# Kernel tuning notes

Measured on AMD Instinct MI355X. Metric: run time of the kernel, lower is better.

The kernel has to match this reference:

```python
import jax, jax.numpy as jnp
import numpy as np

HIDDEN = 2048
HEADS = 16
HEAD_DIM = HIDDEN // HEADS
LATENT = 512
B, T = 2, 2048


def setup_inputs() -> dict:
    key = jax.random.key(0)
    ks = jax.random.split(key, 12)
    s = lambda fan_in: 1.0 / np.sqrt(fan_in)
    x = jax.random.normal(ks[0], (B, T, HIDDEN), dtype=jnp.float32)
    Wq = jax.random.uniform(ks[1], (HIDDEN, HIDDEN), jnp.float32, -s(HIDDEN), s(HIDDEN))
    bq = jax.random.uniform(ks[2], (HIDDEN,), jnp.float32, -s(HIDDEN), s(HIDDEN))
    Wl = jax.random.uniform(ks[3], (HIDDEN, LATENT), jnp.float32, -s(HIDDEN), s(HIDDEN))
    bl = jax.random.uniform(ks[4], (LATENT,), jnp.float32, -s(HIDDEN), s(HIDDEN))
    # per-head back-projections stacked along head axis: [H, latent, head_dim]
    Wk = jax.random.uniform(ks[5], (HEADS, LATENT, HEAD_DIM), jnp.float32, -s(LATENT), s(LATENT))
    bk = jax.random.uniform(ks[6], (HEADS, HEAD_DIM), jnp.float32, -s(LATENT), s(LATENT))
    Wv = jax.random.uniform(ks[7], (HEADS, LATENT, HEAD_DIM), jnp.float32, -s(LATENT), s(LATENT))
    bv = jax.random.uniform(ks[8], (HEADS, HEAD_DIM), jnp.float32, -s(LATENT), s(LATENT))
    Wo = jax.random.uniform(ks[9], (HIDDEN, HIDDEN), jnp.float32, -s(HIDDEN), s(HIDDEN))
    bo = jax.random.uniform(ks[10], (HIDDEN,), jnp.float32, -s(HIDDEN), s(HIDDEN))
    return {"x": x, "Wq": Wq, "bq": bq, "Wl": Wl, "bl": bl,
            "Wk": Wk, "bk": bk, "Wv": Wv, "bv": bv, "Wo": Wo, "bo": bo}


def reference(x, Wq, bq, Wl, bl, Wk, bk, Wv, bv, Wo, bo):
    Bc, Tc, _ = x.shape
    # Q projection, split into heads: [B, H, T, Dh]
    q = (x @ Wq + bq).reshape(Bc, Tc, HEADS, HEAD_DIM).transpose(0, 2, 1, 3)
    # shared low-rank latent KV (cache=None -> just new tokens): [B, T, L]
    latent = x @ Wl + bl
    # per-head back-projections fused as one grouped matmul: [B, H, T, Dh]
    k = jnp.einsum('btl,hld->bhtd', latent, Wk) + bk[None, :, None, :]
    v = jnp.einsum('btl,hld->bhtd', latent, Wv) + bv[None, :, None, :]
    # full (non-causal) attention, matching the original module
    scores = jnp.einsum('bhqd,bhkd->bhqk', q, k) / np.sqrt(HEAD_DIM).astype(jnp.float32)
    probs = jax.nn.softmax(scores, axis=-1)
    attn = jnp.einsum('bhqk,bhkd->bhqd', probs, v)
    attn = attn.transpose(0, 2, 1, 3).reshape(Bc, Tc, HIDDEN)
    return attn @ Wo + bo
```

## Files before the change

### kernel.cpp

```cpp
#include <hip/hip_runtime.h>
#include <hip/hip_bf16.h>
#include <cstdint>

#define SEQ     2048
#define NHID    2048
#define NLAT    512
#define NHEAD   16
#define DHEAD   128
#define NBATCH  2
#define NROWS   (NBATCH*SEQ)

typedef unsigned short u16;
typedef __attribute__((ext_vector_type(8))) short short8;
typedef __attribute__((ext_vector_type(4))) float f32x4;

#define MFMA16 __builtin_amdgcn_mfma_f32_16x16x32_bf16

#define QSCALE 0.12751743f

#if __has_builtin(__builtin_amdgcn_exp2f)
#define EXP2(x) __builtin_amdgcn_exp2f(x)
#else
#define EXP2(x) __expf((x) * 0.6931471805599453f)
#endif

__device__ __forceinline__ u16 f2b(float f) {
    uint32_t u = __float_as_uint(f);
    uint32_t r = (u + 0x7fffu + ((u >> 16) & 1u)) >> 16;
    return (u16)r;
}

__device__ __forceinline__ uint32_t cvt_pk_bf16(float a, float b) {
    uint32_t r;
    asm("v_cvt_pk_bf16_f32 %0, %1, %2" : "=v"(r) : "v"(a), "v"(b));
    return r;
}

__device__ __forceinline__ void async16(const u16* g, u16* l) {
    __builtin_amdgcn_global_load_lds(
        (const __attribute__((address_space(1))) unsigned int*)g,
        (__attribute__((address_space(3))) unsigned int*)l, 16, 0, 0);
}

__device__ __forceinline__ void stage_lds(const u16* __restrict__ src, size_t strideE,
                                          u16* lds, int wave, int lane,
                                          int log2cpr, int xmask, int xshift,
                                          int reps, int nlanes) {
    const int cmask = (1 << log2cpr) - 1;
    for (int rep = 0; rep < reps; ++rep) {
        int cbase = rep * nlanes + wave * 64;
        int ci = cbase + lane;
        int row = ci >> log2cpr;
        int sc = ci & cmask;
        int dchunk = sc ^ ((row >> xshift) & xmask);
        const u16* g = src + (size_t)row * strideE + dchunk * 8;
        async16(g, lds + (size_t)cbase * 8);
    }
}

__global__ __launch_bounds__(256) void prep(const float* __restrict__ x,
                                            const float* __restrict__ Wq,
                                            const float* __restrict__ Wl,
                                            const float* __restrict__ Wk,
                                            const float* __restrict__ Wv,
                                            const float* __restrict__ Wo,
                                            u16* __restrict__ xb,
                                            u16* __restrict__ WqlT,
                                            u16* __restrict__ WkvT,
                                            u16* __restrict__ WoT) {
    const int t = blockIdx.x, tid = threadIdx.x;
    if (t < 8192) {
        int i = t * 256 + tid;
        float4 v = ((const float4*)x)[i];
        unsigned int lo = (unsigned int)f2b(v.x) | ((unsigned int)f2b(v.y) << 16);
        unsigned int hi = (unsigned int)f2b(v.z) | ((unsigned int)f2b(v.w) << 16);
        ((uint2*)xb)[i] = make_uint2(lo, hi);
        return;
    }
    __shared__ float tile[32][33];
    const float* src; u16* dst; int R, C, tY, tX;
    if (t < 12288)      { int tt = t - 8192;  src = Wq; dst = WqlT;           R = 2048; C = 2048; tY = tt >> 6; tX = tt & 63; }
    else if (t < 13312) { int tt = t - 12288; src = Wl; dst = WqlT + 4194304; R = 2048; C = 512;  tY = tt >> 4; tX = tt & 15; }
    else if (t < 14336) { int tt = t - 13312; int hh = tt >> 6; tt &= 63;
                          src = Wk + hh * 65536; dst = WkvT + hh * 65536;     R = 512;  C = 128;  tY = tt >> 2; tX = tt & 3; }
    else if (t < 15360) { int tt = t - 14336; int hh = tt >> 6; tt &= 63;
                          src = Wv + hh * 65536; dst = WkvT + 1048576 + hh * 65536;
                                                                              R = 512;  C = 128;  tY = tt >> 2; tX = tt & 3; }
    else                { int tt = t - 15360; src = Wo; dst = WoT;            R = 2048; C = 2048; tY = tt >> 6; tX = tt & 63; }
    const int r0 = tY * 32, c0 = tX * 32;
    {
        const int rr = tid >> 3, c4 = tid & 7;
        float4 v4 = *(const float4*)&src[(size_t)(r0 + rr) * C + c0 + c4 * 4];
        tile[rr][c4 * 4 + 0] = v4.x;
        tile[rr][c4 * 4 + 1] = v4.y;
        tile[rr][c4 * 4 + 2] = v4.z;
        tile[rr][c4 * 4 + 3] = v4.w;
    }
    __syncthreads();
    {
        const int rg = tid & 7, cc = tid >> 3;
        ushort4 o4;
        o4.x = f2b(tile[rg * 4 + 0][cc]);
        o4.y = f2b(tile[rg * 4 + 1][cc]);
        o4.z = f2b(tile[rg * 4 + 2][cc]);
        o4.w = f2b(tile[rg * 4 + 3][cc]);
        *(ushort4*)&dst[(size_t)(c0 + cc) * R + r0 + rg * 4] = o4;
    }
}

template<int STORE, int BK>
__global__ __launch_bounds__(256) void gemm_bt(const u16* __restrict__ A,
                                               const u16* __restrict__ Bt,
                                               const float* __restrict__ bias1,
                                               const float* __restrict__ bias2,
                                               void* __restrict__ C1,
                                               void* __restrict__ C2,
                                               int M, int N, int K) {
    __shared__ __align__(16) u16 As[2][128 * BK];
    __shared__ __align__(16) u16 Bs[2][128 * BK];
    const int tid = threadIdx.x, wave = tid >> 6, lane = tid & 63;
    const int quad = lane >> 4, m16 = lane & 15;
    const int gx = gridDim.x;
    const int nwg = gx * gridDim.y;
    int lin = blockIdx.x + gx * blockIdx.y;
    int xcd = lin & 7, pos = lin >> 3;
    int qq = nwg >> 3, rr2 = nwg & 7;
    int wg = (xcd < rr2) ? xcd * (qq + 1) + pos
                         : rr2 * (qq + 1) + (xcd - rr2) * qq + pos;
    const int m0 = (wg / gx) * 128, n0 = (wg % gx) * 128;
    const int wr = wave >> 1, wc = wave & 1;
    const u16* Ab = A + (size_t)m0 * K;
    const u16* Bb = Bt + (size_t)n0 * K;
    const int KI = K / BK;

    auto stage = [&](const u16* src, u16* buf) {
        if constexpr (BK == 32) stage_lds(src, K, buf, wave, lane, 2, 3, 1, 2, 256);
        else                    stage_lds(src, K, buf, wave, lane, 3, 7, 0, 4, 256);
    };

    stage(Ab, As[0]);
    stage(Bb, Bs[0]);

    f32x4 acc[4][4] = {};
    for (int it = 0; it < KI; ++it) {
        const int cur = it & 1;
        __syncthreads();
        if (it + 1 < KI) {
            stage(Ab + (it + 1) * BK, As[cur ^ 1]);
            stage(Bb + (it + 1) * BK, Bs[cur ^ 1]);
        }
        if constexpr (BK == 32) {
            const int swz = (quad ^ ((m16 >> 1) & 3)) * 8;
            short8 af[4], bfr[4];
            #pragma unroll
            for (int i = 0; i < 4; i++)
                af[i] = *(const short8*)&As[cur][(wr * 64 + i * 16 + m16) * 32 + swz];
            #pragma unroll
            for (int j = 0; j < 4; j++)
                bfr[j] = *(const short8*)&Bs[cur][(wc * 64 + j * 16 + m16) * 32 + swz];
            #pragma unroll
            for (int i = 0; i < 4; i++)
                #pragma unroll
                for (int j = 0; j < 4; j++)
                    acc[i][j] = MFMA16(af[i], bfr[j], acc[i][j], 0, 0, 0);
        } else {
            #pragma unroll
            for (int kk = 0; kk < 2; kk++) {
                const int swz = ((kk * 4 + quad) ^ (m16 & 7)) * 8;
                short8 af[4], bfr[4];
                #pragma unroll
                for (int i = 0; i < 4; i++)
                    af[i] = *(const short8*)&As[cur][(wr * 64 + i * 16 + m16) * 64 + swz];
                #pragma unroll
                for (int j = 0; j < 4; j++)
                    bfr[j] = *(const short8*)&Bs[cur][(wc * 64 + j * 16 + m16) * 64 + swz];
                #pragma unroll
                for (int i = 0; i < 4; i++)
                    #pragma unroll
                    for (int j = 0; j < 4; j++)
                        acc[i][j] = MFMA16(af[i], bfr[j], acc[i][j], 0, 0, 0);
            }
        }
    }
    const bool second = (n0 >= 2048);
    #pragma unroll
    for (int j = 0; j < 4; j++) {
        int n = n0 + wc * 64 + j * 16 + m16;
        float bv;
        if constexpr (STORE == 2) bv = bias1[n];
        else bv = second ? bias2[n - 2048] : bias1[n];
        #pragma unroll
        for (int i = 0; i < 4; i++) {
            int mrow = m0 + wr * 64 + i * 16 + quad * 4;
            if constexpr (STORE == 4) {
                if (second) {
                    int n2 = n - 2048;
                    ushort4 pkv;
                    pkv.x = f2b(acc[i][j][0] + bv);
                    pkv.y = f2b(acc[i][j][1] + bv);
                    pkv.z = f2b(acc[i][j][2] + bv);
                    pkv.w = f2b(acc[i][j][3] + bv);
                    int c = mrow & 2047;
                    c = (c & ~12) | ((c & 4) << 1) | ((c & 8) >> 1);
                    *(ushort4*)&((u16*)C2)[((size_t)((m0 >> 11) * 2048 + n2)) * 2048 + c] = pkv;
                    continue;
                }
            }
            #pragma unroll
            for (int r = 0; r < 4; r++) {
                float v = acc[i][j][r] + bv;
                int m = mrow + r;
                if constexpr (STORE == 2)
                    ((float*)C1)[(size_t)m * N + n] = v;
                else if constexpr (STORE == 3) {
                    if (!second) ((u16*)C1)[(size_t)m * 2048 + n] = f2b(v * QSCALE);
                    else         ((u16*)C2)[(size_t)m * 512 + (n - 2048)] = f2b(v);
                } else {
                    ((u16*)C1)[(size_t)m * 2048 + n] = f2b(v);
                }
            }
        }
    }
}

__global__ __launch_bounds__(256, 2) void attn_fused(const u16* __restrict__ Q,
                                                     const u16* __restrict__ Kf,
                                                     const u16* __restrict__ Vt,
                                                     u16* __restrict__ Ob) {
    __shared__ __align__(16) u16 Kt[2][64 * 128];
    __shared__ __align__(16) u16 Vtile[2][128 * 64];
    const int tid = threadIdx.x, wave = tid >> 6, lane = tid & 63;
    const int quad = lane >> 4, m16 = lane & 15;
    const int bh = blockIdx.x, b = bh >> 4, h = bh & 15;
    const int q0 = blockIdx.y * 128;
    const size_t grow = (size_t)b * SEQ;
    const u16* Kbase = Kf + grow * NHID + h * DHEAD;
    const u16* Vbase = Vt + (grow + h * DHEAD) * SEQ;

    const u16* qsrc = Q + (grow + q0) * NHID + h * DHEAD;
    stage_lds(qsrc, NHID, Kt[0], wave, lane, 4, 15, 0, 4, 256);
    stage_lds(qsrc + (size_t)64 * NHID, NHID, Kt[1], wave, lane, 4, 15, 0, 4, 256);
    __syncthreads();
    short8 qf[2][4];
    {
        const u16* qbuf = Kt[wave >> 1];
        int rbase = (wave & 1) * 32;
        #pragma unroll
        for (int i = 0; i < 2; i++)
            #pragma unroll
            for (int c = 0; c < 4; c++)
                qf[i][c] = *(const short8*)&qbuf[(rbase + i * 16 + m16) * 128 +
                                                (((c * 4 + quad) ^ m16)) * 8];
    }
    __syncthreads();

    stage_lds(Kbase, NHID, Kt[0], wave, lane, 4, 15, 0, 4, 256);
    stage_lds(Vbase, SEQ, Vtile[0], wave, lane, 3, 7, 0, 4, 256);

    f32x4 o[2][8] = {};
    float lsum[2] = {};

    for (int it = 0; it < SEQ / 64; ++it) {
        const int cur = it & 1;
        __syncthreads();
        if (it + 1 < SEQ / 64) {
            stage_lds(Kbase + (size_t)(it + 1) * 64 * NHID, NHID, Kt[cur ^ 1],
                      wave, lane, 4, 15, 0, 4, 256);
            stage_lds(Vbase + (it + 1) * 64, SEQ, Vtile[cur ^ 1],
                      wave, lane, 3, 7, 0, 4, 256);
        }
        const u16* kt = Kt[cur];
        const u16* vt = Vtile[cur];

        f32x4 s[2][4] = {};
        __builtin_amdgcn_s_setprio(1);
        #pragma unroll
        for (int c = 0; c < 4; c++)
            #pragma unroll
            for (int j = 0; j < 4; j++) {
                short8 kb = *(const short8*)&kt[(j * 16 + m16) * 128 +
                                               (((c * 4 + quad) ^ m16)) * 8];
                s[0][j] = MFMA16(kb, qf[0][c], s[0][j], 0, 0, 0);
                s[1][j] = MFMA16(kb, qf[1][c], s[1][j], 0, 0, 0);
            }
        __builtin_amdgcn_s_setprio(0);

        uint32_t pk[2][4][2];
        #pragma unroll
        for (int i = 0; i < 2; i++) {
            float rs = 0.f;
            #pragma unroll
            for (int j = 0; j < 4; j++) {
                float p0 = EXP2(s[i][j][0]);
                float p1 = EXP2(s[i][j][1]);
                float p2 = EXP2(s[i][j][2]);
                float p3 = EXP2(s[i][j][3]);
                rs += (p0 + p1) + (p2 + p3);
                pk[i][j][0] = cvt_pk_bf16(p0, p1);
                pk[i][j][1] = cvt_pk_bf16(p2, p3);
            }
            lsum[i] += rs;
        }

        __builtin_amdgcn_s_setprio(1);
        #pragma unroll
        for (int c2 = 0; c2 < 2; c2++) {
            short8 pa[2];
            #pragma unroll
            for (int i = 0; i < 2; i++) {
                union { uint32_t u[4]; short8 s8; } pu;
#if __has_builtin(__builtin_amdgcn_permlane32_swap)
                auto r0 = __builtin_amdgcn_permlane32_swap(pk[i][2 * c2][0],
                                                           pk[i][2 * c2 + 1][0],
                                                           false, false);
                auto r1 = __builtin_amdgcn_permlane32_swap(pk[i][2 * c2][1],
                                                           pk[i][2 * c2 + 1][1],
                                                           false, false);
                pu.u[0] = r0[0]; pu.u[1] = r1[0]; pu.u[2] = r0[1]; pu.u[3] = r1[1];
#else
                uint32_t jl0 = pk[i][2 * c2][0],     jl1 = pk[i][2 * c2][1];
                uint32_t jh0 = pk[i][2 * c2 + 1][0], jh1 = pk[i][2 * c2 + 1][1];
                uint32_t sl0 = __shfl_xor(jl0, 32), sl1 = __shfl_xor(jl1, 32);
                uint32_t sh0 = __shfl_xor(jh0, 32), sh1 = __shfl_xor(jh1, 32);
                const bool low = lane < 32;
                pu.u[0] = low ? jl0 : sh0;
                pu.u[1] = low ? jl1 : sh1;
                pu.u[2] = low ? sl0 : jh0;
                pu.u[3] = low ? sl1 : jh1;
#endif
                pa[i] = pu.s8;
            }
            #pragma unroll
            for (int jd = 0; jd < 8; jd++) {
                short8 vb = *(const short8*)&vt[(jd * 16 + m16) * 64 +
                                               (((c2 * 4 + quad) ^ (m16 & 7))) * 8];
                o[0][jd] = MFMA16(pa[0], vb, o[0][jd], 0, 0, 0);
                o[1][jd] = MFMA16(pa[1], vb, o[1][jd], 0, 0, 0);
            }
        }
        __builtin_amdgcn_s_setprio(0);
    }

    #pragma unroll
    for (int i = 0; i < 2; i++) {
        float v = lsum[i];
        v += __shfl_xor(v, 16);
        v += __shfl_xor(v, 32);
        lsum[i] = v;
    }
    #pragma unroll
    for (int i = 0; i < 2; i++) {
        float inv[4];
        #pragma unroll
        for (int r = 0; r < 4; r++)
            inv[r] = 1.f / __shfl(lsum[i], quad * 4 + r);
        #pragma unroll
        for (int jd = 0; jd < 8; jd++)
            #pragma unroll
            for (int r = 0; r < 4; r++) {
                int t = q0 + wave * 32 + i * 16 + quad * 4 + r;
                int d = jd * 16 + m16;
                Ob[(grow + t) * NHID + h * DHEAD + d] = f2b(o[i][jd][r] * inv[r]);
            }
    }
}

extern "C" void kernel_launch(void* const* d_in, const int* in_sizes, int n_in,
                              void* d_out, int out_size, void* d_ws, size_t ws_size,
                              hipStream_t stream) {
    const float* x  = (const float*)d_in[0];
    const float* Wq = (const float*)d_in[1];
    const float* bq = (const float*)d_in[2];
    const float* Wl = (const float*)d_in[3];
    const float* bl = (const float*)d_in[4];
    const float* Wk = (const float*)d_in[5];
    const float* bk = (const float*)d_in[6];
    const float* Wv = (const float*)d_in[7];
    const float* bv = (const float*)d_in[8];
    const float* Wo = (const float*)d_in[9];
    const float* bo = (const float*)d_in[10];
    float* out = (float*)d_out;

    u16* w = (u16*)d_ws;
    u16* xb    = w;
    u16* WqlT  = xb    + 8388608;
    u16* WkvT  = WqlT  + 5242880;
    u16* WoT   = WkvT  + 2097152;
    u16* qb    = WoT   + 4194304;
    u16* kb    = qb    + 8388608;
    u16* vt    = kb    + 8388608;
    u16* lat   = vt    + 8388608;
    u16* attnb = xb;

    prep<<<19456, 256, 0, stream>>>(x, Wq, Wl, Wk, Wv, Wo, xb, WqlT, WkvT, WoT);

    gemm_bt<3, 64><<<dim3(20, 32), 256, 0, stream>>>(xb, WqlT, bq, bl, qb, lat,
                                                     NROWS, 2560, 2048);
    gemm_bt<4, 32><<<dim3(32, 32), 256, 0, stream>>>(lat, WkvT, bk, bv, kb, vt,
                                                     NROWS, 4096, 512);

    attn_fused<<<dim3(32, 16), 256, 0, stream>>>(qb, kb, vt, attnb);

    gemm_bt<2, 64><<<dim3(16, 32), 256, 0, stream>>>(attnb, WoT, bo, nullptr, out, nullptr,
                                                     NROWS, 2048, 2048);
}
```

Before: 335.4 us.

## Halve attention tiles to 64 queries and 32 keys for higher occupancy

The attention kernel now gives each wave 16 query rows instead of 32 and streams 32-key tiles instead of 64. This halves register and LDS use, raises launch bounds to 4 blocks per CU and doubles the grid, with the V-tile swizzle adjusted to the new 32-wide layout. The cost is half the MFMA work per K/V tile load, so K/V traffic per query doubles and the kernel does twice as many barriers. Separately, the QKV GEMM's second template parameter changes from 64 to 32.

```diff
diff --git a/kernel.cpp b/kernel.cpp
--- a/kernel.cpp
+++ b/kernel.cpp
@@ -223,146 +223,128 @@
     }
 }
 
-__global__ __launch_bounds__(256, 2) void attn_fused(const u16* __restrict__ Q,
+__global__ __launch_bounds__(256, 4) void attn_fused(const u16* __restrict__ Q,
                                                      const u16* __restrict__ Kf,
                                                      const u16* __restrict__ Vt,
                                                      u16* __restrict__ Ob) {
-    __shared__ __align__(16) u16 Kt[2][64 * 128];
-    __shared__ __align__(16) u16 Vtile[2][128 * 64];
+    __shared__ __align__(16) u16 Kt[2][32 * 128];
+    __shared__ __align__(16) u16 Vtile[2][128 * 32];
     const int tid = threadIdx.x, wave = tid >> 6, lane = tid & 63;
     const int quad = lane >> 4, m16 = lane & 15;
     const int bh = blockIdx.x, b = bh >> 4, h = bh & 15;
-    const int q0 = blockIdx.y * 128;
+    const int q0 = blockIdx.y * 64;
     const size_t grow = (size_t)b * SEQ;
     const u16* Kbase = Kf + grow * NHID + h * DHEAD;
     const u16* Vbase = Vt + (grow + h * DHEAD) * SEQ;
 
     const u16* qsrc = Q + (grow + q0) * NHID + h * DHEAD;
-    stage_lds(qsrc, NHID, Kt[0], wave, lane, 4, 15, 0, 4, 256);
-    stage_lds(qsrc + (size_t)64 * NHID, NHID, Kt[1], wave, lane, 4, 15, 0, 4, 256);
+    stage_lds(qsrc, NHID, Kt[0], wave, lane, 4, 15, 0, 2, 256);
+    stage_lds(qsrc + (size_t)32 * NHID, NHID, Kt[1], wave, lane, 4, 15, 0, 2, 256);
     __syncthreads();
-    short8 qf[2][4];
+    short8 qf[4];
     {
         const u16* qbuf = Kt[wave >> 1];
-        int rbase = (wave & 1) * 32;
-        #pragma unroll
-        for (int i = 0; i < 2; i++)
-            #pragma unroll
-            for (int c = 0; c < 4; c++)
-                qf[i][c] = *(const short8*)&qbuf[(rbase + i * 16 + m16) * 128 +
-                                                (((c * 4 + quad) ^ m16)) * 8];
+        int rbase = (wave & 1) * 16;
+        #pragma unroll
+        for (int c = 0; c < 4; c++)
+            qf[c] = *(const short8*)&qbuf[(rbase + m16) * 128 +
+                                          (((c * 4 + quad) ^ m16)) * 8];
     }
     __syncthreads();
 
-    stage_lds(Kbase, NHID, Kt[0], wave, lane, 4, 15, 0, 4, 256);
-    stage_lds(Vbase, SEQ, Vtile[0], wave, lane, 3, 7, 0, 4, 256);
-
-    f32x4 o[2][8] = {};
-    float lsum[2] = {};
-
-    for (int it = 0; it < SEQ / 64; ++it) {
+    stage_lds(Kbase, NHID, Kt[0], wave, lane, 4, 15, 0, 2, 256);
+    stage_lds(Vbase, SEQ, Vtile[0], wave, lane, 2, 3, 1, 2, 256);
+
+    f32x4 o[8] = {};
+    float lsum = 0.f;
+
+    for (int it = 0; it < SEQ / 32; ++it) {
         const int cur = it & 1;
         __syncthreads();
-        if (it + 1 < SEQ / 64) {
-            stage_lds(Kbase + (size_t)(it + 1) * 64 * NHID, NHID, Kt[cur ^ 1],
-                      wave, lane, 4, 15, 0, 4, 256);
-            stage_lds(Vbase + (it + 1) * 64, SEQ, Vtile[cur ^ 1],
-                      wave, lane, 3, 7, 0, 4, 256);
+        if (it + 1 < SEQ / 32) {
+            stage_lds(Kbase + (size_t)(it + 1) * 32 * NHID, NHID, Kt[cur ^ 1],
+                      wave, lane, 4, 15, 0, 2, 256);
+            stage_lds(Vbase + (it + 1) * 32, SEQ, Vtile[cur ^ 1],
+                      wave, lane, 2, 3, 1, 2, 256);
         }
         const u16* kt = Kt[cur];
         const u16* vt = Vtile[cur];
 
-        f32x4 s[2][4] = {};
+        f32x4 s[2] = {};
         __builtin_amdgcn_s_setprio(1);
         #pragma unroll
         for (int c = 0; c < 4; c++)
             #pragma unroll
-            for (int j = 0; j < 4; j++) {
+            for (int j = 0; j < 2; j++) {
                 short8 kb = *(const short8*)&kt[(j * 16 + m16) * 128 +
                                                (((c * 4 + quad) ^ m16)) * 8];
-                s[0][j] = MFMA16(kb, qf[0][c], s[0][j], 0, 0, 0);
-                s[1][j] = MFMA16(kb, qf[1][c], s[1][j], 0, 0, 0);
+                s[j] = MFMA16(kb, qf[c], s[j], 0, 0, 0);
             }
         __builtin_amdgcn_s_setprio(0);
 
-        uint32_t pk[2][4][2];
-        #pragma unroll
-        for (int i = 0; i < 2; i++) {
-            float rs = 0.f;
-            #pragma unroll
-            for (int j = 0; j < 4; j++) {
-                float p0 = EXP2(s[i][j][0]);
-                float p1 = EXP2(s[i][j][1]);
-                float p2 = EXP2(s[i][j][2]);
-                float p3 = EXP2(s[i][j][3]);
-                rs += (p0 + p1) + (p2 + p3);
-                pk[i][j][0] = cvt_pk_bf16(p0, p1);
-                pk[i][j][1] = cvt_pk_bf16(p2, p3);
-            }
-            lsum[i] += rs;
+        uint32_t pk0[2], pk1[2];
+        {
+            float p0 = EXP2(s[0][0]);
+            float p1 = EXP2(s[0][1]);
+            float p2 = EXP2(s[0][2]);
+            float p3 = EXP2(s[0][3]);
+            float p4 = EXP2(s[1][0]);
+            float p5 = EXP2(s[1][1]);
+            float p6 = EXP2(s[1][2]);
+            float p7 = EXP2(s[1][3]);
+            lsum += ((p0 + p1) + (p2 + p3)) + ((p4 + p5) + (p6 + p7));
+            pk0[0] = cvt_pk_bf16(p0, p1);
+            pk0[1] = cvt_pk_bf16(p2, p3);
+            pk1[0] = cvt_pk_bf16(p4, p5);
+            pk1[1] = cvt_pk_bf16(p6, p7);
         }
 
         __builtin_amdgcn_s_setprio(1);
-        #pragma unroll
-        for (int c2 = 0; c2 < 2; c2++) {
-            short8 pa[2];
-            #pragma unroll
-            for (int i = 0; i < 2; i++) {
-                union { uint32_t u[4]; short8 s8; } pu;
+        short8 pa;
+        {
+            union { uint32_t u[4]; short8 s8; } pu;
 #if __has_builtin(__builtin_amdgcn_permlane32_swap)
-                auto r0 = __builtin_amdgcn_permlane32_swap(pk[i][2 * c2][0],
-                                                           pk[i][2 * c2 + 1][0],
-                                                           false, false);
-                auto r1 = __builtin_amdgcn_permlane32_swap(pk[i][2 * c2][1],
-                                                           pk[i][2 * c2 + 1][1],
-                                                           false, false);
-                pu.u[0] = r0[0]; pu.u[1] = r1[0]; pu.u[2] = r0[1]; pu.u[3] = r1[1];
+            auto r0 = __builtin_amdgcn_permlane32_swap(pk0[0], pk1[0], false, false);
+            auto r1 = __builtin_amdgcn_permlane32_swap(pk0[1], pk1[1], false, false);
+            pu.u[0] = r0[0]; pu.u[1] = r1[0]; pu.u[2] = r0[1]; pu.u[3] = r1[1];
 #else
-                uint32_t jl0 = pk[i][2 * c2][0],     jl1 = pk[i][2 * c2][1];
-                uint32_t jh0 = pk[i][2 * c2 + 1][0], jh1 = pk[i][2 * c2 + 1][1];
-                uint32_t sl0 = __shfl_xor(jl0, 32), sl1 = __shfl_xor(jl1, 32);
-                uint32_t sh0 = __shfl_xor(jh0, 32), sh1 = __shfl_xor(jh1, 32);
-                const bool low = lane < 32;
-                pu.u[0] = low ? jl0 : sh0;
-                pu.u[1] = low ? jl1 : sh1;
-                pu.u[2] = low ? sl0 : jh0;
-                pu.u[3] = low ? sl1 : jh1;
+            uint32_t sl0 = __shfl_xor(pk0[0], 32), sl1 = __shfl_xor(pk0[1], 32);
+            uint32_t sh0 = __shfl_xor(pk1[0], 32), sh1 = __shfl_xor(pk1[1], 32);
+            const bool low = lane < 32;
+            pu.u[0] = low ? pk0[0] : sh0;
+            pu.u[1] = low ? pk0[1] : sh1;
+            pu.u[2] = low ? sl0 : pk1[0];
+            pu.u[3] = low ? sl1 : pk1[1];
 #endif
-                pa[i] = pu.s8;
-            }
-            #pragma unroll
-            for (int jd = 0; jd < 8; jd++) {
-                short8 vb = *(const short8*)&vt[(jd * 16 + m16) * 64 +
-                                               (((c2 * 4 + quad) ^ (m16 & 7))) * 8];
-                o[0][jd] = MFMA16(pa[0], vb, o[0][jd], 0, 0, 0);
-                o[1][jd] = MFMA16(pa[1], vb, o[1][jd], 0, 0, 0);
-            }
+            pa = pu.s8;
+        }
+        #pragma unroll
+        for (int jd = 0; jd < 8; jd++) {
+            short8 vb = *(const short8*)&vt[(jd * 16 + m16) * 32 +
+                                           ((quad ^ ((m16 >> 1) & 3))) * 8];
+            o[jd] = MFMA16(pa, vb, o[jd], 0, 0, 0);
         }
         __builtin_amdgcn_s_setprio(0);
     }
 
-    #pragma unroll
-    for (int i = 0; i < 2; i++) {
-        float v = lsum[i];
+    {
+        float v = lsum;
         v += __shfl_xor(v, 16);
         v += __shfl_xor(v, 32);
-        lsum[i] = v;
-    }
+        lsum = v;
+    }
+    float inv[4];
     #pragma unroll
-    for (int i = 0; i < 2; i++) {
-        float inv[4];
-        #pragma unroll
-        for (int r = 0; r < 4; r++)
-            inv[r] = 1.f / __shfl(lsum[i], quad * 4 + r);
-        #pragma unroll
-        for (int jd = 0; jd < 8; jd++)
-            #pragma unroll
-            for (int r = 0; r < 4; r++) {
-                int t = q0 + wave * 32 + i * 16 + quad * 4 + r;
-                int d = jd * 16 + m16;
-                Ob[(grow + t) * NHID + h * DHEAD + d] = f2b(o[i][jd][r] * inv[r]);
-            }
-    }
+    for (int r = 0; r < 4; r++)
+        inv[r] = 1.f / __shfl(lsum, quad * 4 + r);
+    #pragma unroll
+    for (int jd = 0; jd < 8; jd++)
+        #pragma unroll
+        for (int r = 0; r < 4; r++) {
+            int t = q0 + wave * 16 + quad * 4 + r;
+            int d = jd * 16 + m16;
+            Ob[(grow + t) * NHID + h * DHEAD + d] = f2b(o[jd][r] * inv[r]);
+        }
 }
 
 extern "C" void kernel_launch(void* const* d_in, const int* in_sizes, int n_in,
@@ -394,12 +376,12 @@
 
     prep<<<19456, 256, 0, stream>>>(x, Wq, Wl, Wk, Wv, Wo, xb, WqlT, WkvT, WoT);
 
-    gemm_bt<3, 64><<<dim3(20, 32), 256, 0, stream>>>(xb, WqlT, bq, bl, qb, lat,
+    gemm_bt<3, 32><<<dim3(20, 32), 256, 0, stream>>>(xb, WqlT, bq, bl, qb, lat,
                                                      NROWS, 2560, 2048);
     gemm_bt<4, 32><<<dim3(32, 32), 256, 0, stream>>>(lat, WkvT, bk, bv, kb, vt,
                                                      NROWS, 4096, 512);
 
-    attn_fused<<<dim3(32, 16), 256, 0, stream>>>(qb, kb, vt, attnb);
+    attn_fused<<<dim3(32, 32), 256, 0, stream>>>(qb, kb, vt, attnb);
 
     gemm_bt<2, 64><<<dim3(16, 32), 256, 0, stream>>>(attnb, WoT, bo, nullptr, out, nullptr,
                                                      NROWS, 2048, 2048);
```

New measurement: 328.3 us. 2.1% less time.
